# Kernel optimization log

Measured on AMD Instinct MI355X. Metric: run time of the kernel, lower is better.

The kernel has to match this reference:

```python
import jax, jax.numpy as jnp
import numpy as np

NEG = -1e30  # safe log-zero (avoids inf arithmetic under jit)
EPS = 1e-7   # keras backend epsilon used by ctc_batch_cost


def _ctc_batch_cost(y_true, y_pred, label_length):
    """Faithful jax port of tf.keras.backend.ctc_batch_cost with
    input_length == T for all examples (as in CTCLayer.call).
    y_true: [B, L] int labels (blank excluded), y_pred: [B, T, C] probs,
    label_length: [B, 1] int. Returns loss [B, 1]. Blank index = C - 1.
    """
    B, T, C = y_pred.shape
    L = y_true.shape[1]
    S = 2 * L + 1  # extended label length (blanks interleaved)
    blank = C - 1
    ll = jnp.squeeze(label_length, axis=-1).astype(jnp.int32)  # [B]

    logp = jnp.log(y_pred + EPS)  # [B, T, C]

    # Pad labels beyond label_length with blank so the repeat-skip test is safe.
    lab = jnp.where(jnp.arange(L)[None, :] < ll[:, None], y_true, blank)  # [B, L]
    ext = jnp.full((B, S), blank, dtype=lab.dtype).at[:, 1::2].set(lab)   # [B, S]

    # Gather per-state log-probs: lp_ext[b, t, s] = logp[b, t, ext[b, s]]
    lp_ext = jnp.take_along_axis(
        logp, jnp.broadcast_to(ext[:, None, :], (B, T, S)), axis=2)  # [B, T, S]

    # Skip transition s-2 -> s allowed iff ext[s] is a label and differs from ext[s-2].
    ext_m2 = jnp.concatenate(
        [jnp.full((B, 2), blank, dtype=ext.dtype), ext[:, :-2]], axis=1)
    allow_skip = (ext != blank) & (ext != ext_m2)  # [B, S]

    # alpha[0]: only states 0 (blank) and 1 (first label) are reachable.
    alpha0 = jnp.where(jnp.arange(S)[None, :] < 2, lp_ext[:, 0, :], NEG)  # [B, S]

    negcol1 = jnp.full((B, 1), NEG, dtype=logp.dtype)
    negcol2 = jnp.full((B, 2), NEG, dtype=logp.dtype)

    def step(alpha, lp_t):
        a0 = alpha                                                   # stay
        a1 = jnp.concatenate([negcol1, alpha[:, :-1]], axis=1)      # s-1 -> s
        a2 = jnp.where(allow_skip,
                       jnp.concatenate([negcol2, alpha[:, :-2]], axis=1),
                       NEG)                                          # s-2 -> s
        m = jnp.maximum(jnp.maximum(a0, a1), a2)
        new = m + jnp.log(jnp.exp(a0 - m) + jnp.exp(a1 - m) + jnp.exp(a2 - m)) + lp_t
        return new, None

    lp_rest = jnp.swapaxes(lp_ext[:, 1:, :], 0, 1)  # [T-1, B, S] time-major
    alpha_T, _ = jax.lax.scan(step, alpha0, lp_rest)  # [B, S]

    # Valid endings: final blank (s = 2*ll) or final label (s = 2*ll - 1).
    a_blank = jnp.take_along_axis(alpha_T, (2 * ll)[:, None], axis=1)[:, 0]
    a_label = jnp.take_along_axis(alpha_T, (2 * ll - 1)[:, None], axis=1)[:, 0]
    m = jnp.maximum(a_blank, a_label)
    log_lik = m + jnp.log(jnp.exp(a_blank - m) + jnp.exp(a_label - m))
    return -log_lik[:, None]  # [B, 1]


def setup_inputs() -> dict:
    key = jax.random.key(0)
    k1, k2, k3 = jax.random.split(key, 3)
    B, T, C, L = 64, 128, 4000, 48
    logits = jax.random.normal(k1, (B, T, C), dtype=jnp.float32)
    y_pred = jax.nn.softmax(logits, axis=-1)  # module expects probabilities
    y_true = jax.random.randint(k2, (B, L), 0, C - 1, dtype=jnp.int32)  # blank excluded
    label_length = jax.random.randint(k3, (B, 1), 1, L + 1, dtype=jnp.int32)
    return {"y_true": y_true, "y_pred": y_pred, "label_length": label_length}


def reference(y_true, y_pred, label_length):
    # CTCLayer.call returns y_pred and registers the loss via add_loss; the
    # kernel-relevant computation is the CTC loss itself, returned here.
    return _ctc_batch_cost(y_true, y_pred, label_length)
```

## Files before the change

kernel.cpp:

```cpp
#include <hip/hip_runtime.h>
#include <math.h>


#define NEGV (-1e30f)
#define EPSV (1e-7f)

constexpr int B = 64, T = 128, C = 4000, L = 48;
constexpr int BLANK = C - 1;
constexpr int NCLS = L + 1;
constexpr int TOTAL = B * T * NCLS;

#if __has_builtin(__builtin_amdgcn_exp2f)
__device__ __forceinline__ float fexp2(float x) { return __builtin_amdgcn_exp2f(x); }
#else
__device__ __forceinline__ float fexp2(float x) { return exp2f(x); }
#endif
#if __has_builtin(__builtin_amdgcn_logf)
__device__ __forceinline__ float flog2(float x) { return __builtin_amdgcn_logf(x); }
#else
__device__ __forceinline__ float flog2(float x) { return log2f(x); }
#endif

__device__ __forceinline__ float dpp_shr1_neg(float x) {
    int r = __builtin_amdgcn_update_dpp(__float_as_int(NEGV), __float_as_int(x),
                                        0x138 , 0xF, 0xF, false);
    return __int_as_float(r);
}

__global__ __launch_bounds__(256) void gather_kernel(
    const int* __restrict__ y_true,
    const float* __restrict__ y_pred,
    const int* __restrict__ label_len,
    float* __restrict__ lp_ws)
{
    const int base = blockIdx.x * 256;
    const int tid  = threadIdx.x;
    const int idx  = base + tid;

    const int b0 = base / (T * NCLS);
    const int b1 = (base + 255) / (T * NCLS);

    __shared__ int cls_s[2 * NCLS];
    __shared__ int ll_sh[2];

    if (tid < NCLS) {
        int ll = label_len[b0];
        if (tid == 0) ll_sh[0] = ll;
        int cls = BLANK;
        if (tid < L) cls = (tid < ll) ? y_true[b0 * L + tid] : BLANK;
        cls_s[tid] = cls;
    } else if (tid >= 128 && tid < 128 + NCLS) {
        int j = tid - 128;
        int ll = label_len[b1];
        if (j == 0) ll_sh[1] = ll;
        int cls = BLANK;
        if (j < L) cls = (j < ll) ? y_true[b1 * L + j] : BLANK;
        cls_s[NCLS + j] = cls;
    }
    __syncthreads();

    int bt = idx / NCLS;
    int j  = idx - bt * NCLS;
    int b  = bt >> 7;
    int rb = b - b0;

    if (j >= ll_sh[rb] && j < L) return;

    int cls = cls_s[rb * NCLS + j];
    float p = y_pred[(size_t)bt * C + cls];
    lp_ws[idx] = flog2(p + EPSV);
}

__global__ __launch_bounds__(256) void dp_kernel(
    const int* __restrict__ y_true,
    const int* __restrict__ label_len,
    const float* __restrict__ lp_ws,
    float* __restrict__ out)
{
    const int b = blockIdx.x;
    const int tid = threadIdx.x;

    __shared__ float lp_s[T * NCLS + 32];
    __shared__ int   lab_s[L];
    __shared__ int   ll_s;

    if (tid < L) {
        int ll = label_len[b];
        if (tid == 0) ll_s = ll;
        int v = y_true[b * L + tid];
        lab_s[tid] = (tid < ll) ? v : BLANK;
    }

    const float4* src = (const float4*)(lp_ws + (size_t)b * T * NCLS);
    float4* dst = (float4*)lp_s;
    for (int i = tid; i < (T * NCLS) / 4; i += 256) dst[i] = src[i];
    __syncthreads();

    if (tid >= 64) return;
    const int lane = tid;
    const int ll = ll_s;

    const int myLab   = (lane < L) ? lab_s[lane] : BLANK;
    const int prevLab = (lane >= 1 && lane - 1 < L) ? lab_s[lane - 1] : BLANK;
    const bool allow2 = (lane >= 1) && (myLab != BLANK) && (myLab != prevLab);

    float a0 = (lane == 0) ? lp_s[48] : NEGV;
    float a1 = (lane == 0) ? lp_s[0]  : NEGV;

    float lpb_n = lp_s[1 * NCLS + 48];
    float lpl_n = (lane < L) ? lp_s[1 * NCLS + lane] : 0.0f;

    for (int t = 1; t < T; ++t) {
        float lpb = lpb_n, lpl = lpl_n;
        int tn = (t + 1 < T) ? t + 1 : t;
        lpb_n = lp_s[tn * NCLS + 48];
        lpl_n = (lane < L) ? lp_s[tn * NCLS + lane] : 0.0f;

        float pa1 = dpp_shr1_neg(a1);

        float m0 = fmaxf(a0, pa1);
        float n0 = fminf(a0, pa1);
        float r0 = (m0 + lpb) + flog2(1.0f + fexp2(n0 - m0));

        float c12 = allow2 ? pa1 : NEGV;
        float m1 = fmaxf(fmaxf(a1, a0), c12);
        float r1 = (m1 + lpl) + flog2(fexp2(a1 - m1) + fexp2(a0 - m1) +
                                      fexp2(c12 - m1));

        a0 = r0;
        a1 = (lane < L) ? r1 : NEGV;
    }

    float ab = __shfl(a0, ll);
    float al = __shfl(a1, ll - 1);
    if (lane == 0) {
        float m = fmaxf(ab, al);
        float ll2 = m + flog2(fexp2(ab - m) + fexp2(al - m));
        out[b] = -ll2 * 0.69314718055994531f;
    }
}

__global__ __launch_bounds__(256) void ctc_fused_kernel(
    const int* __restrict__ y_true,
    const float* __restrict__ y_pred,
    const int* __restrict__ label_len,
    float* __restrict__ out)
{
    const int b = blockIdx.x;
    const int tid = threadIdx.x;

    __shared__ float lp_s[T * NCLS + 32];
    __shared__ int   lab_s[L];
    __shared__ int   ll_s;

    if (tid < L) {
        int ll = label_len[b];
        if (tid == 0) ll_s = ll;
        int v = y_true[b * L + tid];
        lab_s[tid] = (tid < ll) ? v : BLANK;
    }
    __syncthreads();

    const float* yp = y_pred + (size_t)b * T * C;
    for (int g = tid; g < T * NCLS; g += 256) {
        int t = g / NCLS;
        int j = g - t * NCLS;
        int cls = (j < L) ? lab_s[j] : BLANK;
        lp_s[g] = flog2(yp[t * C + cls] + EPSV);
    }
    __syncthreads();

    if (tid >= 64) return;
    const int lane = tid;
    const int ll = ll_s;
    const int myLab   = (lane < L) ? lab_s[lane] : BLANK;
    const int prevLab = (lane >= 1 && lane - 1 < L) ? lab_s[lane - 1] : BLANK;
    const bool allow2 = (lane >= 1) && (myLab != BLANK) && (myLab != prevLab);

    float a0 = (lane == 0) ? lp_s[48] : NEGV;
    float a1 = (lane == 0) ? lp_s[0]  : NEGV;

    for (int t = 1; t < T; ++t) {
        float lpb = lp_s[t * NCLS + 48];
        float lpl = (lane < L) ? lp_s[t * NCLS + lane] : 0.0f;

        float pa1 = dpp_shr1_neg(a1);

        float m0 = fmaxf(a0, pa1);
        float n0 = fminf(a0, pa1);
        float r0 = (m0 + lpb) + flog2(1.0f + fexp2(n0 - m0));

        float c12 = allow2 ? pa1 : NEGV;
        float m1 = fmaxf(fmaxf(a1, a0), c12);
        float r1 = (m1 + lpl) + flog2(fexp2(a1 - m1) + fexp2(a0 - m1) +
                                      fexp2(c12 - m1));

        a0 = r0;
        a1 = (lane < L) ? r1 : NEGV;
    }

    float ab = __shfl(a0, ll);
    float al = __shfl(a1, ll - 1);
    if (lane == 0) {
        float m = fmaxf(ab, al);
        float ll2 = m + flog2(fexp2(ab - m) + fexp2(al - m));
        out[b] = -ll2 * 0.69314718055994531f;
    }
}

extern "C" void kernel_launch(void* const* d_in, const int* in_sizes, int n_in,
                              void* d_out, int out_size, void* d_ws, size_t ws_size,
                              hipStream_t stream) {
    const int*   y_true       = (const int*)d_in[0];
    const float* y_pred       = (const float*)d_in[1];
    const int*   label_length = (const int*)d_in[2];
    float*       out          = (float*)d_out;

    const size_t need = (size_t)TOTAL * sizeof(float);
    if (ws_size >= need) {
        float* lp_ws = (float*)d_ws;
        gather_kernel<<<TOTAL / 256, 256, 0, stream>>>(
            y_true, y_pred, label_length, lp_ws);
        dp_kernel<<<B, 256, 0, stream>>>(y_true, label_length, lp_ws, out);
    } else {
        ctc_fused_kernel<<<B, 256, 0, stream>>>(y_true, y_pred, label_length, out);
    }
}
```

Before: 23.10 us.

## Merge gather and DP into one cooperative kernel with grid sync

Replaces the two-kernel gather-then-DP sequence with a single cooperative launch of 256 blocks. Each block first gathers log-probs into the workspace using a strided loop, then a grid-wide sync runs, and the first B blocks perform the DP. This removes one kernel launch and its inter-kernel gap, at the cost of grid-sync overhead and a much smaller grid for the gather phase. The fallback path now reuses the workspace instead of the fused single-kernel version, which looks inconsistent when the workspace is too small.

```diff
diff --git a/kernel.cpp b/kernel.cpp
--- a/kernel.cpp
+++ b/kernel.cpp
@@ -1,5 +1,8 @@
 #include <hip/hip_runtime.h>
+#include <hip/hip_cooperative_groups.h>
 #include <math.h>
+
+namespace cg = cooperative_groups;
 
 
 #define NEGV (-1e30f)
@@ -27,66 +30,17 @@
     return __int_as_float(r);
 }
 
-__global__ __launch_bounds__(256) void gather_kernel(
-    const int* __restrict__ y_true,
-    const float* __restrict__ y_pred,
-    const int* __restrict__ label_len,
-    float* __restrict__ lp_ws)
-{
-    const int base = blockIdx.x * 256;
-    const int tid  = threadIdx.x;
-    const int idx  = base + tid;
-
-    const int b0 = base / (T * NCLS);
-    const int b1 = (base + 255) / (T * NCLS);
-
-    __shared__ int cls_s[2 * NCLS];
-    __shared__ int ll_sh[2];
-
-    if (tid < NCLS) {
-        int ll = label_len[b0];
-        if (tid == 0) ll_sh[0] = ll;
-        int cls = BLANK;
-        if (tid < L) cls = (tid < ll) ? y_true[b0 * L + tid] : BLANK;
-        cls_s[tid] = cls;
-    } else if (tid >= 128 && tid < 128 + NCLS) {
-        int j = tid - 128;
-        int ll = label_len[b1];
-        if (j == 0) ll_sh[1] = ll;
-        int cls = BLANK;
-        if (j < L) cls = (j < ll) ? y_true[b1 * L + j] : BLANK;
-        cls_s[NCLS + j] = cls;
-    }
-    __syncthreads();
-
-    int bt = idx / NCLS;
-    int j  = idx - bt * NCLS;
-    int b  = bt >> 7;
-    int rb = b - b0;
-
-    if (j >= ll_sh[rb] && j < L) return;
-
-    int cls = cls_s[rb * NCLS + j];
-    float p = y_pred[(size_t)bt * C + cls];
-    lp_ws[idx] = flog2(p + EPSV);
-}
-
-__global__ __launch_bounds__(256) void dp_kernel(
+__device__ __forceinline__ void dp_body(
+    int b, int tid,
     const int* __restrict__ y_true,
     const int* __restrict__ label_len,
     const float* __restrict__ lp_ws,
-    float* __restrict__ out)
+    float* __restrict__ out,
+    float* lp_s , int* lab_s , int* ll_sp)
 {
-    const int b = blockIdx.x;
-    const int tid = threadIdx.x;
-
-    __shared__ float lp_s[T * NCLS + 32];
-    __shared__ int   lab_s[L];
-    __shared__ int   ll_s;
-
     if (tid < L) {
         int ll = label_len[b];
-        if (tid == 0) ll_s = ll;
+        if (tid == 0) *ll_sp = ll;
         int v = y_true[b * L + tid];
         lab_s[tid] = (tid < ll) ? v : BLANK;
     }
@@ -98,7 +52,7 @@
 
     if (tid >= 64) return;
     const int lane = tid;
-    const int ll = ll_s;
+    const int ll = *ll_sp;
 
     const int myLab   = (lane < L) ? lab_s[lane] : BLANK;
     const int prevLab = (lane >= 1 && lane - 1 < L) ? lab_s[lane - 1] : BLANK;
@@ -140,72 +94,76 @@
     }
 }
 
-__global__ __launch_bounds__(256) void ctc_fused_kernel(
+__global__ __launch_bounds__(256) void ctc_coop(
     const int* __restrict__ y_true,
     const float* __restrict__ y_pred,
     const int* __restrict__ label_len,
+    float* __restrict__ lp_ws,
     float* __restrict__ out)
 {
-    const int b = blockIdx.x;
     const int tid = threadIdx.x;
+    const int blk = blockIdx.x;
 
     __shared__ float lp_s[T * NCLS + 32];
     __shared__ int   lab_s[L];
     __shared__ int   ll_s;
 
-    if (tid < L) {
-        int ll = label_len[b];
-        if (tid == 0) ll_s = ll;
-        int v = y_true[b * L + tid];
-        lab_s[tid] = (tid < ll) ? v : BLANK;
-    }
-    __syncthreads();
-
-    const float* yp = y_pred + (size_t)b * T * C;
-    for (int g = tid; g < T * NCLS; g += 256) {
-        int t = g / NCLS;
-        int j = g - t * NCLS;
-        int cls = (j < L) ? lab_s[j] : BLANK;
-        lp_s[g] = flog2(yp[t * C + cls] + EPSV);
-    }
-    __syncthreads();
-
-    if (tid >= 64) return;
-    const int lane = tid;
-    const int ll = ll_s;
-    const int myLab   = (lane < L) ? lab_s[lane] : BLANK;
-    const int prevLab = (lane >= 1 && lane - 1 < L) ? lab_s[lane - 1] : BLANK;
-    const bool allow2 = (lane >= 1) && (myLab != BLANK) && (myLab != prevLab);
-
-    float a0 = (lane == 0) ? lp_s[48] : NEGV;
-    float a1 = (lane == 0) ? lp_s[0]  : NEGV;
-
-    for (int t = 1; t < T; ++t) {
-        float lpb = lp_s[t * NCLS + 48];
-        float lpl = (lane < L) ? lp_s[t * NCLS + lane] : 0.0f;
-
-        float pa1 = dpp_shr1_neg(a1);
-
-        float m0 = fmaxf(a0, pa1);
-        float n0 = fminf(a0, pa1);
-        float r0 = (m0 + lpb) + flog2(1.0f + fexp2(n0 - m0));
-
-        float c12 = allow2 ? pa1 : NEGV;
-        float m1 = fmaxf(fmaxf(a1, a0), c12);
-        float r1 = (m1 + lpl) + flog2(fexp2(a1 - m1) + fexp2(a0 - m1) +
-                                      fexp2(c12 - m1));
-
-        a0 = r0;
-        a1 = (lane < L) ? r1 : NEGV;
+    const int gbase = blk * 256 + tid;
+    #pragma unroll
+    for (int k = 0; k < 7; ++k) {
+        int idx = gbase + k * 65536;
+        if (idx < TOTAL) {
+            int bt = idx / NCLS;
+            int j  = idx - bt * NCLS;
+            int b  = bt >> 7;
+            int cls = BLANK;
+            if (j < L) {
+                int ll = label_len[b];
+                cls = (j < ll) ? y_true[b * L + j] : BLANK;
+            }
+            float p = y_pred[(size_t)bt * C + cls];
+            lp_ws[idx] = flog2(p + EPSV);
+        }
     }
 
-    float ab = __shfl(a0, ll);
-    float al = __shfl(a1, ll - 1);
-    if (lane == 0) {
-        float m = fmaxf(ab, al);
-        float ll2 = m + flog2(fexp2(ab - m) + fexp2(al - m));
-        out[b] = -ll2 * 0.69314718055994531f;
+    __threadfence();
+    cg::this_grid().sync();
+
+    if (blk >= B) return;
+    dp_body(blk, tid, y_true, label_len, lp_ws, out, lp_s, lab_s, &ll_s);
+}
+
+__global__ __launch_bounds__(256) void gather_kernel(
+    const int* __restrict__ y_true,
+    const float* __restrict__ y_pred,
+    const int* __restrict__ label_len,
+    float* __restrict__ lp_ws)
+{
+    int idx = blockIdx.x * 256 + threadIdx.x;
+    if (idx >= TOTAL) return;
+    int bt = idx / NCLS;
+    int j  = idx - bt * NCLS;
+    int b  = bt >> 7;
+    int cls = BLANK;
+    if (j < L) {
+        int ll = label_len[b];
+        cls = (j < ll) ? y_true[b * L + j] : BLANK;
     }
+    float p = y_pred[(size_t)bt * C + cls];
+    lp_ws[idx] = flog2(p + EPSV);
+}
+
+__global__ __launch_bounds__(256) void dp_kernel(
+    const int* __restrict__ y_true,
+    const int* __restrict__ label_len,
+    const float* __restrict__ lp_ws,
+    float* __restrict__ out)
+{
+    __shared__ float lp_s[T * NCLS + 32];
+    __shared__ int   lab_s[L];
+    __shared__ int   ll_s;
+    dp_body(blockIdx.x, threadIdx.x, y_true, label_len, lp_ws, out,
+            lp_s, lab_s, &ll_s);
 }
 
 extern "C" void kernel_launch(void* const* d_in, const int* in_sizes, int n_in,
@@ -219,10 +177,14 @@
     const size_t need = (size_t)TOTAL * sizeof(float);
     if (ws_size >= need) {
         float* lp_ws = (float*)d_ws;
-        gather_kernel<<<TOTAL / 256, 256, 0, stream>>>(
+        void* args[] = { (void*)&y_true, (void*)&y_pred, (void*)&label_length,
+                         (void*)&lp_ws, (void*)&out };
+        hipLaunchCooperativeKernel(reinterpret_cast<void*>(ctc_coop),
+                                   dim3(256), dim3(256), args, 0, stream);
+    } else {
+        float* lp_ws = (float*)d_ws;
+        gather_kernel<<<(TOTAL + 255) / 256, 256, 0, stream>>>(
             y_true, y_pred, label_length, lp_ws);
         dp_kernel<<<B, 256, 0, stream>>>(y_true, label_length, lp_ws, out);
-    } else {
-        ctc_fused_kernel<<<B, 256, 0, stream>>>(y_true, y_pred, label_length, out);
     }
 }
```

Result: slower. 84.00 us (+263.7%).

## Overlap DP recurrence with chunked shared-memory loads in dp kernel

Applied to the files above, without the earlier changes.

The dp kernel now loads only the first two of eight time-chunks before starting the recurrence. Warps 1-3 stream later chunks into shared memory while warp 0 runs the alpha recursion over 16 timesteps per phase, with a block barrier between phases. This hides the global-to-LDS copy latency behind the serial DP. The gather kernel also drops its early-exit for padded label positions, so every element is gathered and written, which removes the branch but adds some extra loads. The eight per-phase barriers add synchronisation cost.

```diff
diff --git a/kernel.cpp b/kernel.cpp
--- a/kernel.cpp
+++ b/kernel.cpp
@@ -8,7 +8,9 @@
 constexpr int B = 64, T = 128, C = 4000, L = 48;
 constexpr int BLANK = C - 1;
 constexpr int NCLS = L + 1;
-constexpr int TOTAL = B * T * NCLS;
+constexpr int SLICE = T * NCLS;
+constexpr int TOTAL = B * SLICE;
+constexpr int CH_F4 = 196;
 
 #if __has_builtin(__builtin_amdgcn_exp2f)
 __device__ __forceinline__ float fexp2(float x) { return __builtin_amdgcn_exp2f(x); }
@@ -37,22 +39,19 @@
     const int tid  = threadIdx.x;
     const int idx  = base + tid;
 
-    const int b0 = base / (T * NCLS);
-    const int b1 = (base + 255) / (T * NCLS);
+    const int b0 = base / SLICE;
+    const int b1 = (base + 255) / SLICE;
 
     __shared__ int cls_s[2 * NCLS];
-    __shared__ int ll_sh[2];
 
     if (tid < NCLS) {
         int ll = label_len[b0];
-        if (tid == 0) ll_sh[0] = ll;
         int cls = BLANK;
         if (tid < L) cls = (tid < ll) ? y_true[b0 * L + tid] : BLANK;
         cls_s[tid] = cls;
     } else if (tid >= 128 && tid < 128 + NCLS) {
         int j = tid - 128;
         int ll = label_len[b1];
-        if (j == 0) ll_sh[1] = ll;
         int cls = BLANK;
         if (j < L) cls = (j < ll) ? y_true[b1 * L + j] : BLANK;
         cls_s[NCLS + j] = cls;
@@ -62,11 +61,7 @@
     int bt = idx / NCLS;
     int j  = idx - bt * NCLS;
     int b  = bt >> 7;
-    int rb = b - b0;
-
-    if (j >= ll_sh[rb] && j < L) return;
-
-    int cls = cls_s[rb * NCLS + j];
+    int cls = cls_s[(b - b0) * NCLS + j];
     float p = y_pred[(size_t)bt * C + cls];
     lp_ws[idx] = flog2(p + EPSV);
 }
@@ -80,9 +75,12 @@
     const int b = blockIdx.x;
     const int tid = threadIdx.x;
 
-    __shared__ float lp_s[T * NCLS + 32];
+    __shared__ float lp_s[SLICE + 32];
     __shared__ int   lab_s[L];
     __shared__ int   ll_s;
+
+    const float4* src = (const float4*)(lp_ws + (size_t)b * SLICE);
+    float4* dst = (float4*)lp_s;
 
     if (tid < L) {
         int ll = label_len[b];
@@ -91,52 +89,68 @@
         lab_s[tid] = (tid < ll) ? v : BLANK;
     }
 
-    const float4* src = (const float4*)(lp_ws + (size_t)b * T * NCLS);
-    float4* dst = (float4*)lp_s;
-    for (int i = tid; i < (T * NCLS) / 4; i += 256) dst[i] = src[i];
-    __syncthreads();
-
-    if (tid >= 64) return;
+    for (int i = tid; i < 2 * CH_F4; i += 256) dst[i] = src[i];
+    __syncthreads();
+
     const int lane = tid;
-    const int ll = ll_s;
-
-    const int myLab   = (lane < L) ? lab_s[lane] : BLANK;
-    const int prevLab = (lane >= 1 && lane - 1 < L) ? lab_s[lane - 1] : BLANK;
-    const bool allow2 = (lane >= 1) && (myLab != BLANK) && (myLab != prevLab);
-
-    float a0 = (lane == 0) ? lp_s[48] : NEGV;
-    float a1 = (lane == 0) ? lp_s[0]  : NEGV;
-
-    float lpb_n = lp_s[1 * NCLS + 48];
-    float lpl_n = (lane < L) ? lp_s[1 * NCLS + lane] : 0.0f;
-
-    for (int t = 1; t < T; ++t) {
-        float lpb = lpb_n, lpl = lpl_n;
-        int tn = (t + 1 < T) ? t + 1 : t;
-        lpb_n = lp_s[tn * NCLS + 48];
-        lpl_n = (lane < L) ? lp_s[tn * NCLS + lane] : 0.0f;
-
-        float pa1 = dpp_shr1_neg(a1);
-
-        float m0 = fmaxf(a0, pa1);
-        float n0 = fminf(a0, pa1);
-        float r0 = (m0 + lpb) + flog2(1.0f + fexp2(n0 - m0));
-
-        float c12 = allow2 ? pa1 : NEGV;
-        float m1 = fmaxf(fmaxf(a1, a0), c12);
-        float r1 = (m1 + lpl) + flog2(fexp2(a1 - m1) + fexp2(a0 - m1) +
-                                      fexp2(c12 - m1));
-
-        a0 = r0;
-        a1 = (lane < L) ? r1 : NEGV;
-    }
-
-    float ab = __shfl(a0, ll);
-    float al = __shfl(a1, ll - 1);
-    if (lane == 0) {
-        float m = fmaxf(ab, al);
-        float ll2 = m + flog2(fexp2(ab - m) + fexp2(al - m));
-        out[b] = -ll2 * 0.69314718055994531f;
+    int myLab = BLANK, prevLab = BLANK;
+    bool allow2 = false;
+    float a0 = NEGV, a1 = NEGV, lpb_n = 0.0f, lpl_n = 0.0f;
+    int lidx = 48, ll = 1;
+    if (tid < 64) {
+        ll = ll_s;
+        myLab   = (lane < L) ? lab_s[lane] : BLANK;
+        prevLab = (lane >= 1 && lane - 1 < L) ? lab_s[lane - 1] : BLANK;
+        allow2 = (lane >= 1) && (myLab != BLANK) && (myLab != prevLab);
+        a0 = (lane == 0) ? lp_s[48] : NEGV;
+        a1 = (lane == 0) ? lp_s[0]  : NEGV;
+        lidx = (lane < NCLS) ? lane : 48;
+        lpb_n = lp_s[1 * NCLS + 48];
+        lpl_n = (lane < L) ? lp_s[1 * NCLS + lidx] : 0.0f;
+    }
+
+    for (int p = 0; p < 8; ++p) {
+        if (tid >= 64) {
+            int cs = p + 2;
+            if (cs < 8) {
+                for (int i = cs * CH_F4 + (tid - 64); i < (cs + 1) * CH_F4; i += 192)
+                    dst[i] = src[i];
+            }
+        } else {
+            int t0 = (p == 0) ? 1 : 16 * p;
+            int t1 = 16 * p + 15;
+            for (int t = t0; t <= t1; ++t) {
+                float lpb = lpb_n, lpl = lpl_n;
+                int tn = (t + 1 < T) ? t + 1 : t;
+                lpb_n = lp_s[tn * NCLS + 48];
+                lpl_n = (lane < L) ? lp_s[tn * NCLS + lidx] : 0.0f;
+
+                float pa1 = dpp_shr1_neg(a1);
+
+                float m0 = fmaxf(a0, pa1);
+                float n0 = fminf(a0, pa1);
+                float r0 = (m0 + lpb) + flog2(1.0f + fexp2(n0 - m0));
+
+                float c12 = allow2 ? pa1 : NEGV;
+                float m1 = fmaxf(fmaxf(a1, a0), c12);
+                float r1 = (m1 + lpl) + flog2(fexp2(a1 - m1) + fexp2(a0 - m1) +
+                                              fexp2(c12 - m1));
+
+                a0 = r0;
+                a1 = (lane < L) ? r1 : NEGV;
+            }
+        }
+        __syncthreads();
+    }
+
+    if (tid < 64) {
+        float ab = __shfl(a0, ll);
+        float al = __shfl(a1, ll - 1);
+        if (lane == 0) {
+            float m = fmaxf(ab, al);
+            float ll2 = m + flog2(fexp2(ab - m) + fexp2(al - m));
+            out[b] = -ll2 * 0.69314718055994531f;
+        }
     }
 }
 
@@ -149,7 +163,7 @@
     const int b = blockIdx.x;
     const int tid = threadIdx.x;
 
-    __shared__ float lp_s[T * NCLS + 32];
+    __shared__ float lp_s[SLICE + 32];
     __shared__ int   lab_s[L];
     __shared__ int   ll_s;
 
@@ -162,7 +176,7 @@
     __syncthreads();
 
     const float* yp = y_pred + (size_t)b * T * C;
-    for (int g = tid; g < T * NCLS; g += 256) {
+    for (int g = tid; g < SLICE; g += 256) {
         int t = g / NCLS;
         int j = g - t * NCLS;
         int cls = (j < L) ? lab_s[j] : BLANK;
```

Result: slower. 26.27 us (+13.8%).
